# Optimization experiments

Measured on AMD Instinct MI355X. Metric: run time of the kernel, lower is better.

Reference implementation:

```python
import jax, jax.numpy as jnp
import numpy as np
import math

D_MODEL = 1024
NUM_HEADS = 16
SEQ = 2048
BATCH = 4


def setup_inputs() -> dict:
    key = jax.random.key(0)
    ks = jax.random.split(key, 7)
    s = 0.02
    return {
        "x": jax.random.normal(ks[0], (BATCH, SEQ, D_MODEL), jnp.float32),
        "Wq": jax.random.normal(ks[1], (D_MODEL, D_MODEL), jnp.float32) * s,
        "bq": jax.random.normal(ks[2], (D_MODEL,), jnp.float32) * s,
        "Wkv": jax.random.normal(ks[3], (D_MODEL, 2 * D_MODEL), jnp.float32) * s,
        "bkv": jax.random.normal(ks[4], (2 * D_MODEL,), jnp.float32) * s,
        "Wo": jax.random.normal(ks[5], (D_MODEL, D_MODEL), jnp.float32) * s,
        "bo": jax.random.normal(ks[6], (D_MODEL,), jnp.float32) * s,
        "decoderMask": 1,
    }


def reference(x, Wq, bq, Wkv, bkv, Wo, bo, decoderMask):
    B, S, D = x.shape
    H = NUM_HEADS
    dh = D // H
    q_ = x @ Wq + bq              # [B,S,D]
    kv_ = x @ Wkv + bkv           # [B,S,2D] (self-attention: m is None)
    # Faithful to source: concat [q_, kv_] then reshape into heads of 3*dh,
    # which interleaves Q/KV projection columns across heads.
    qkv = jnp.concatenate([q_, kv_], axis=-1)          # [B,S,3D]
    qkv = qkv.reshape(B, S, H, 3 * dh).transpose(0, 2, 1, 3)  # [B,H,S,3dh]
    q, k, v = jnp.split(qkv, 3, axis=-1)               # each [B,H,S,dh]
    scaled = jnp.einsum("bhqd,bhkd->bhqk", q, k) / math.sqrt(dh)
    if decoderMask:
        mask = jnp.triu(jnp.full((S, S), -jnp.inf, dtype=scaled.dtype), k=1)
        scaled = scaled + mask
    attn = jax.nn.softmax(scaled, axis=-1)
    vals = jnp.einsum("bhqk,bhkd->bhqd", attn, v)      # [B,H,S,dh]
    vals = vals.transpose(0, 2, 1, 3).reshape(B, S, D)
    return vals @ Wo + bo
```

## Files before the change

### kernel.cpp

```cpp
#include <hip/hip_runtime.h>
#include <cstddef>
#include <cstdint>

#define SEQ   2048
#define BATCH 4
#define DM    1024
#define NH    16
#define DH    64
#define ROWS  (BATCH*SEQ)
#define NC3   3072
#define SM_SCALE 0.18033688f

typedef unsigned short u16;
typedef __attribute__((ext_vector_type(8))) short bf16x8;
typedef __attribute__((ext_vector_type(2))) float f32x2;
typedef __attribute__((ext_vector_type(4))) float f32x4;
typedef __attribute__((ext_vector_type(16))) float f32x16;
typedef __attribute__((ext_vector_type(4))) unsigned u32x4;
typedef __attribute__((ext_vector_type(2))) unsigned u32x2;

union V16 { f32x16 v; f32x2 p[8]; };

__device__ __forceinline__ u16 f2b(float f) {
  union { float f; unsigned u; } v; v.f = f;
  unsigned r = v.u + 0x7fffu + ((v.u >> 16) & 1u);
  return (u16)(r >> 16);
}

__device__ __forceinline__ unsigned cvt_pk_bf16(float lo, float hi) {
  unsigned r;
  asm("v_cvt_pk_bf16_f32 %0, %1, %2" : "=v"(r) : "v"(lo), "v"(hi));
  return r;
}

__device__ __forceinline__ void plswap(unsigned& a, unsigned& b) {
  auto rr = __builtin_amdgcn_permlane32_swap((int)a, (int)b, false, false);
  a = (unsigned)rr[0];
  b = (unsigned)rr[1];
}

__device__ __forceinline__ float ex2(float x) { return __builtin_amdgcn_exp2f(x); }

__device__ __forceinline__ void gld16(const void* g, void* l) {
  __builtin_amdgcn_global_load_lds((const __attribute__((address_space(1))) void*)g,
                                   (__attribute__((address_space(3))) void*)l,
                                   16, 0, 0);
}

__global__ __launch_bounds__(256) void prep_tw_kernel(
    const float* __restrict__ x, const float* __restrict__ bq,
    const float* __restrict__ bkv, u16* __restrict__ xb, float* __restrict__ bc,
    const float* __restrict__ Wq, const float* __restrict__ Wkv,
    const float* __restrict__ Wo, u16* __restrict__ Wt)
{
  __shared__ float t_[32][33];
  const int tid = threadIdx.x;
  if (blockIdx.x < 8192) {
    int i = blockIdx.x * 256 + tid;
    int idx = i * 4;
    float4 v = *(const float4*)(x + idx);
    xb[idx + 0] = f2b(v.x);
    xb[idx + 1] = f2b(v.y);
    xb[idx + 2] = f2b(v.z);
    xb[idx + 3] = f2b(v.w);
    if (i < NC3) bc[i] = (i < DM) ? bq[i] : bkv[i - DM];
  } else {
    const int bid = blockIdx.x - 8192;
    const int n0 = (bid & 127) * 32, k0 = (bid >> 7) * 32;
    const int xcol = tid & 31, yrow = tid >> 5;
    #pragma unroll
    for (int it = 0; it < 4; ++it) {
      int k = k0 + yrow + it * 8;
      int n = n0 + xcol;
      float v;
      if (n < DM)           v = Wq[k * DM + n];
      else if (n < NC3)     v = Wkv[k * (2 * DM) + (n - DM)];
      else                  v = Wo[k * DM + (n - NC3)];
      t_[yrow + it * 8][xcol] = v;
    }
    __syncthreads();
    #pragma unroll
    for (int it = 0; it < 4; ++it) {
      int n = n0 + yrow + it * 8;
      int k = k0 + xcol;
      Wt[(size_t)n * DM + k] = f2b(t_[xcol][yrow + it * 8]);
    }
  }
}

template <int MODE>
__global__ __launch_bounds__(256) void gemm_bt(
    const u16* __restrict__ A, const u16* __restrict__ Bt,
    const float* __restrict__ bias, void* __restrict__ C,
    u16* __restrict__ Vt, int M, int N, int K)
{
  __shared__ alignas(16) u16 lds_[3 * 8192];
  const int tid = threadIdx.x;
  const int lane = tid & 63, wid = tid >> 6;
  const int wr = (wid >> 1) * 64, wc = (wid & 1) * 64;
  const int l15 = lane & 15, lhi = lane >> 4;

  const int bid = blockIdx.x;
  const int xcd = bid & 7, t = bid >> 3;
  const int rsub = t & 7, colb = t >> 3;
  const int row0 = (xcd * 8 + rsub) * 128, col0 = colb * 128;
  const int sr = tid >> 2, scol = (tid & 3) * 8;

  const u16* aS0 = A  + (size_t)(row0 + sr) * K + scol;
  const u16* aS1 = A  + (size_t)(row0 + 64 + sr) * K + scol;
  const u16* bS0 = Bt + (size_t)(col0 + sr) * K + scol;
  const u16* bS1 = Bt + (size_t)(col0 + 64 + sr) * K + scol;
  const int dA = tid * 8;

  int aoff[4], boff[4];
  #pragma unroll
  for (int m = 0; m < 4; ++m) aoff[m] = (wr + m * 16 + l15) * 32 + lhi * 8;
  #pragma unroll
  for (int n = 0; n < 4; ++n) boff[n] = 4096 + (wc + n * 16 + l15) * 32 + lhi * 8;

  f32x4 acc[4][4];
  #pragma unroll
  for (int m = 0; m < 4; ++m)
    #pragma unroll
    for (int n = 0; n < 4; ++n) { f32x4 z = {0.f, 0.f, 0.f, 0.f}; acc[m][n] = z; }

  const int KT = K >> 5;

  auto stage = [&](int kt, u16* base) {
    const int ka = kt * 32;
    gld16(aS0 + ka, base + dA);
    gld16(aS1 + ka, base + 2048 + dA);
    gld16(bS0 + ka, base + 4096 + dA);
    gld16(bS1 + ka, base + 6144 + dA);
  };

  u16* const bufA = lds_;
  u16* const bufB = lds_ + 8192;
  u16* const bufC = lds_ + 16384;

  stage(0, bufA); stage(1, bufB);
  asm volatile("s_waitcnt vmcnt(4)" ::: "memory");
  __builtin_amdgcn_s_barrier();

  u16* rb = bufA;
  u16* sb = bufC;
  for (int kt = 0; kt < KT; ++kt) {
    bf16x8 a[4], b[4];
    #pragma unroll
    for (int m = 0; m < 4; ++m) a[m] = *(const bf16x8*)&rb[aoff[m]];
    #pragma unroll
    for (int n = 0; n < 4; ++n) b[n] = *(const bf16x8*)&rb[boff[n]];
    if (kt + 2 < KT) stage(kt + 2, sb);
    __builtin_amdgcn_s_setprio(1);
    #pragma unroll
    for (int m = 0; m < 4; ++m)
      #pragma unroll
      for (int n = 0; n < 4; ++n)
        acc[m][n] = __builtin_amdgcn_mfma_f32_16x16x32_bf16(a[m], b[n], acc[m][n], 0, 0, 0);
    __builtin_amdgcn_s_setprio(0);
    if (kt + 1 < KT) {
      if (kt + 2 < KT) { asm volatile("s_waitcnt vmcnt(4)" ::: "memory"); }
      else             { asm volatile("s_waitcnt vmcnt(0)" ::: "memory"); }
      __builtin_amdgcn_s_barrier();
    }
    rb = (rb == bufC) ? bufA : rb + 8192;
    sb = (sb == bufC) ? bufA : sb + 8192;
  }

  #pragma unroll
  for (int m = 0; m < 4; ++m)
    #pragma unroll
    for (int n = 0; n < 4; ++n) {
      const int col = col0 + wc + n * 16 + l15;
      const float bv = bias[col];
      if (MODE == 0) {
        #pragma unroll
        for (int r = 0; r < 4; ++r) {
          const int row = row0 + wr + m * 16 + lhi * 4 + r;
          ((float*)C)[(size_t)row * N + col] = acc[m][n][r] + bv;
        }
      } else {
        const int hh = col / 192;
        const int cc = col - hh * 192;
        if (cc < 128) {
          const float qs = (cc < 64) ? SM_SCALE : 1.f;
          #pragma unroll
          for (int r = 0; r < 4; ++r) {
            const int row = row0 + wr + m * 16 + lhi * 4 + r;
            ((u16*)C)[(size_t)row * N + col] = f2b((acc[m][n][r] + bv) * qs);
          }
        } else {
          u16 wv[4];
          #pragma unroll
          for (int r = 0; r < 4; ++r) wv[r] = f2b(acc[m][n][r] + bv);
          const int row = row0 + wr + m * 16 + lhi * 4;
          const int bb = row >> 11, j = row & (SEQ - 1);
          u16* vt = Vt + ((size_t)(bb * NH + hh) * 64 + (cc - 128)) * SEQ + j;
          u32x2 pv = { (unsigned)wv[0] | ((unsigned)wv[1] << 16),
                       (unsigned)wv[2] | ((unsigned)wv[3] << 16) };
          *(u32x2*)vt = pv;
        }
      }
    }
}

__global__ __launch_bounds__(256) void attn_kernel(
    const u16* __restrict__ qkv, const u16* __restrict__ Vt, u16* __restrict__ ctx)
{
  const int bid = blockIdx.x;
  const int p   = (bid >> 3) & 7;
  const int g   = (bid & 7) + ((bid >> 6) << 3);
  const int h   = g & 15, b = g >> 4;
  const int tid = threadIdx.x;
  const int lane = tid & 63, wid = tid >> 6;
  const int l31 = lane & 31, lhi5 = lane >> 5;

  __shared__ alignas(16) u16 smem[8192 + 3 * 8192];
  u16* const Qs = smem;
  u16* const R0 = smem + 8192;
  u16* const R1 = R0 + 8192;
  u16* const R2 = R1 + 8192;

  const size_t kv_row = (size_t)(b * NH + h) * 64;
  const int sr = tid >> 3, sck = tid & 7;
  const int scks = sck ^ (sr & 7);

  const u16* kBase = qkv + (size_t)(b * SEQ + sr) * NC3 + h * 192 + 64 + scks * 8;
  const u16* vBase = Vt + (kv_row + sr) * SEQ + scks * 8;
  const size_t kRow32 = (size_t)32 * NC3;
  const size_t vRow32 = (size_t)32 * SEQ;
  const int dOff0 = sr * 64 + sck * 8;
  const int dOff1 = (32 + sr) * 64 + sck * 8;

  int koff[4], koff2[4];
  #pragma unroll
  for (int c = 0; c < 4; ++c) {
    koff[c]  = l31 * 64        + (((2 * c + lhi5) ^ (l31 & 7)) * 8);
    koff2[c] = (32 + l31) * 64 + (((2 * c + lhi5) ^ (l31 & 7)) * 8);
  }

  #pragma unroll 1
  for (int half = 0; half < 2; ++half) {
    const int qt = half ? (7 - p) : (8 + p);
    const int q0 = qt * 128;
    const int nt = qt * 2 + 2;

    #pragma unroll
    for (int it = 0; it < 4; ++it) {
      int row = it * 32 + sr;
      gld16(qkv + (size_t)(b * SEQ + q0 + row) * NC3 + h * 192 + scks * 8,
            Qs + row * 64 + sck * 8);
    }
    {
      const u16* ks = kBase;          const u16* vs = vBase;
      gld16(ks,          R0 + dOff0); gld16(ks + kRow32, R0 + dOff1);
      gld16(vs,          R0 + 4096 + dOff0); gld16(vs + vRow32, R0 + 4096 + dOff1);
      ks = kBase + (size_t)64 * NC3;  vs = vBase + 64;
      gld16(ks,          R1 + dOff0); gld16(ks + kRow32, R1 + dOff1);
      gld16(vs,          R1 + 4096 + dOff0); gld16(vs + vRow32, R1 + 4096 + dOff1);
    }
    asm volatile("s_waitcnt vmcnt(4)" ::: "memory");
    __builtin_amdgcn_s_barrier();

    bf16x8 qf[4];
    {
      const int qrow = wid * 32 + l31;
      #pragma unroll
      for (int c = 0; c < 4; ++c)
        qf[c] = *(const bf16x8*)&Qs[qrow * 64 + (((2 * c + lhi5) ^ (qrow & 7)) * 8)];
    }

    V16 o0, o1;
    #pragma unroll
    for (int r = 0; r < 16; ++r) { o0.v[r] = 0.f; o1.v[r] = 0.f; }
    float lrow = 0.f;

    const int qw0 = q0 + wid * 32;
    const int qa  = qw0 + l31;
    const int dqb = qa - 4 * lhi5;

    u16* rb = R0;
    u16* sb = R2;
    for (int jt = 0; jt < nt; ++jt) {
      const int j0 = jt * 64;

      if (jt + 2 < nt) {
        const u16* ks = kBase + (size_t)(j0 + 128) * NC3;
        const u16* vs = vBase + (j0 + 128);
        gld16(ks,          sb + dOff0); gld16(ks + kRow32, sb + dOff1);
        gld16(vs,          sb + 4096 + dOff0); gld16(vs + vRow32, sb + 4096 + dOff1);
      }

      if (j0 <= qw0 + 31) {
        const u16* Kb = rb;
        const u16* Vb = rb + 4096;
        V16 s0, s1;
        #pragma unroll
        for (int r = 0; r < 16; ++r) { s0.v[r] = 0.f; s1.v[r] = 0.f; }
        __builtin_amdgcn_s_setprio(1);
        #pragma unroll
        for (int c = 0; c < 4; ++c) {
          bf16x8 kf = *(const bf16x8*)&Kb[koff[c]];
          s0.v = __builtin_amdgcn_mfma_f32_32x32x16_bf16(kf, qf[c], s0.v, 0, 0, 0);
        }
        #pragma unroll
        for (int c = 0; c < 4; ++c) {
          bf16x8 kf = *(const bf16x8*)&Kb[koff2[c]];
          s1.v = __builtin_amdgcn_mfma_f32_32x32x16_bf16(kf, qf[c], s1.v, 0, 0, 0);
        }
        __builtin_amdgcn_s_setprio(0);

        if (j0 + 63 > qw0) {
          const int dq = dqb - j0;
          #pragma unroll
          for (int r = 0; r < 16; ++r) {
            const int kvc = (r & 3) + 8 * (r >> 2);
            s0.v[r] = (kvc > dq)      ? -1e30f : s0.v[r];
            s1.v[r] = (kvc + 32 > dq) ? -1e30f : s1.v[r];
          }
        }

        f32x2 sum2 = {0.f, 0.f};
        #pragma unroll
        for (int i = 0; i < 8; ++i) {
          f32x2 e0, e1;
          e0[0] = ex2(s0.p[i][0]); e0[1] = ex2(s0.p[i][1]);
          e1[0] = ex2(s1.p[i][0]); e1[1] = ex2(s1.p[i][1]);
          s0.p[i] = e0; s1.p[i] = e1;
          sum2 += e0 + e1;
        }
        float ps = sum2[0] + sum2[1];
        {
          unsigned a = __builtin_bit_cast(unsigned, ps), bb = a;
          plswap(a, bb);
          ps = __builtin_bit_cast(float, a) + __builtin_bit_cast(float, bb);
        }
        lrow += ps;

        unsigned pk0[8], pk1[8];
        #pragma unroll
        for (int i = 0; i < 4; ++i) {
          pk0[2 * i]     = cvt_pk_bf16(s0.v[4 * i + 0], s0.v[4 * i + 1]);
          pk0[2 * i + 1] = cvt_pk_bf16(s0.v[4 * i + 2], s0.v[4 * i + 3]);
          pk1[2 * i]     = cvt_pk_bf16(s1.v[4 * i + 0], s1.v[4 * i + 1]);
          pk1[2 * i + 1] = cvt_pk_bf16(s1.v[4 * i + 2], s1.v[4 * i + 3]);
        }
        bf16x8 pf[4];
        {
          unsigned a0 = pk0[0], b0 = pk0[2]; plswap(a0, b0);
          unsigned a1 = pk0[1], b1 = pk0[3]; plswap(a1, b1);
          u32x4 w0v = {a0, a1, b0, b1}; pf[0] = __builtin_bit_cast(bf16x8, w0v);
          unsigned a2 = pk0[4], b2 = pk0[6]; plswap(a2, b2);
          unsigned a3 = pk0[5], b3 = pk0[7]; plswap(a3, b3);
          u32x4 w1v = {a2, a3, b2, b3}; pf[1] = __builtin_bit_cast(bf16x8, w1v);
          unsigned a4 = pk1[0], b4 = pk1[2]; plswap(a4, b4);
          unsigned a5 = pk1[1], b5 = pk1[3]; plswap(a5, b5);
          u32x4 w2v = {a4, a5, b4, b5}; pf[2] = __builtin_bit_cast(bf16x8, w2v);
          unsigned a6 = pk1[4], b6 = pk1[6]; plswap(a6, b6);
          unsigned a7 = pk1[5], b7 = pk1[7]; plswap(a7, b7);
          u32x4 w3v = {a6, a7, b6, b7}; pf[3] = __builtin_bit_cast(bf16x8, w3v);
        }

        __builtin_amdgcn_s_setprio(1);
        #pragma unroll
        for (int c = 0; c < 4; ++c) {
          bf16x8 vf = *(const bf16x8*)&Vb[koff[c]];
          o0.v = __builtin_amdgcn_mfma_f32_32x32x16_bf16(vf, pf[c], o0.v, 0, 0, 0);
        }
        #pragma unroll
        for (int c = 0; c < 4; ++c) {
          bf16x8 vf = *(const bf16x8*)&Vb[koff2[c]];
          o1.v = __builtin_amdgcn_mfma_f32_32x32x16_bf16(vf, pf[c], o1.v, 0, 0, 0);
        }
        __builtin_amdgcn_s_setprio(0);
      }

      if (jt + 2 < nt)      { asm volatile("s_waitcnt vmcnt(4)" ::: "memory"); }
      else if (jt + 1 < nt) { asm volatile("s_waitcnt vmcnt(0)" ::: "memory"); }
      __builtin_amdgcn_s_barrier();
      rb = (rb == R2) ? R0 : rb + 8192;
      sb = (sb == R2) ? R0 : sb + 8192;
    }

    const float inv = 1.f / lrow;
    u16* crow = ctx + (size_t)(b * SEQ + qa) * DM + h * DH;
    #pragma unroll
    for (int i = 0; i < 4; ++i) {
      u32x2 v0, v1;
      v0[0] = cvt_pk_bf16(o0.v[4 * i + 0] * inv, o0.v[4 * i + 1] * inv);
      v0[1] = cvt_pk_bf16(o0.v[4 * i + 2] * inv, o0.v[4 * i + 3] * inv);
      v1[0] = cvt_pk_bf16(o1.v[4 * i + 0] * inv, o1.v[4 * i + 1] * inv);
      v1[1] = cvt_pk_bf16(o1.v[4 * i + 2] * inv, o1.v[4 * i + 3] * inv);
      *(u32x2*)&crow[8 * i + 4 * lhi5]      = v0;
      *(u32x2*)&crow[32 + 8 * i + 4 * lhi5] = v1;
    }
  }
}

extern "C" void kernel_launch(void* const* d_in, const int* in_sizes, int n_in,
                              void* d_out, int out_size, void* d_ws, size_t ws_size,
                              hipStream_t stream) {
  (void)in_sizes; (void)n_in; (void)out_size; (void)ws_size;
  const float* x   = (const float*)d_in[0];
  const float* Wq  = (const float*)d_in[1];
  const float* bq  = (const float*)d_in[2];
  const float* Wkv = (const float*)d_in[3];
  const float* bkv = (const float*)d_in[4];
  const float* Wo  = (const float*)d_in[5];
  const float* bo  = (const float*)d_in[6];
  float* out = (float*)d_out;

  char* w = (char*)d_ws;
  size_t off = 0;
  auto alloc = [&](size_t bytes) { void* p = w + off; off += (bytes + 255) & ~(size_t)255; return p; };
  u16*   xb   = (u16*)alloc((size_t)ROWS * DM * 2);
  u16*   qkvb = (u16*)alloc((size_t)ROWS * NC3 * 2);
  u16*   Vt   = (u16*)alloc((size_t)BATCH * NH * DH * SEQ * 2);
  u16*   Wt   = (u16*)alloc((size_t)4096 * DM * 2);
  float* bc   = (float*)alloc((size_t)NC3 * 4);
  u16*   ctx  = xb;

  prep_tw_kernel<<<dim3(8192 + 4096), 256, 0, stream>>>(x, bq, bkv, xb, bc, Wq, Wkv, Wo, Wt);
  gemm_bt<1><<<dim3((ROWS / 128) * (NC3 / 128)), 256, 0, stream>>>(xb, Wt, bc, qkvb, Vt, ROWS, NC3, DM);
  attn_kernel<<<dim3(512), 256, 0, stream>>>(qkvb, Vt, ctx);
  gemm_bt<0><<<dim3((ROWS / 128) * (DM / 128)), 256, 0, stream>>>(ctx, Wt + (size_t)NC3 * DM, bo, out, nullptr, ROWS, DM, DM);
}
```

Before: 162.3 us.

## Software-pipeline QK^T one tile ahead with a four-deep K/V ring

Grows the LDS K/V ring from three to four stages and prefetches three tiles ahead. It also computes the next tile's QK^T scores before the current tile's softmax and PV MFMAs, so matrix work can overlap the exp and pack instructions. The goal is to hide global-load latency and the dependency stall between score MFMAs and softmax. In exchange it uses more LDS, which may cut occupancy, and holds extra score registers, which may raise VGPR pressure.

```diff
diff --git a/kernel.cpp b/kernel.cpp
--- a/kernel.cpp
+++ b/kernel.cpp
@@ -215,11 +215,9 @@
   const int lane = tid & 63, wid = tid >> 6;
   const int l31 = lane & 31, lhi5 = lane >> 5;
 
-  __shared__ alignas(16) u16 smem[8192 + 3 * 8192];
-  u16* const Qs = smem;
-  u16* const R0 = smem + 8192;
-  u16* const R1 = R0 + 8192;
-  u16* const R2 = R1 + 8192;
+  __shared__ alignas(16) u16 smem[8192 + 4 * 8192];
+  u16* const Qs   = smem;
+  u16* const Ring = smem + 8192;
 
   const size_t kv_row = (size_t)(b * NH + h) * 64;
   const int sr = tid >> 3, sck = tid & 7;
@@ -239,6 +237,16 @@
     koff2[c] = (32 + l31) * 64 + (((2 * c + lhi5) ^ (l31 & 7)) * 8);
   }
 
+  auto stageKV = [&](int jt) {
+    u16* base = Ring + (jt & 3) * 8192;
+    const u16* ks = kBase + (size_t)(jt * 64) * NC3;
+    const u16* vs = vBase + jt * 64;
+    gld16(ks,          base + dOff0);
+    gld16(ks + kRow32, base + dOff1);
+    gld16(vs,          base + 4096 + dOff0);
+    gld16(vs + vRow32, base + 4096 + dOff1);
+  };
+
   #pragma unroll 1
   for (int half = 0; half < 2; ++half) {
     const int qt = half ? (7 - p) : (8 + p);
@@ -251,15 +259,9 @@
       gld16(qkv + (size_t)(b * SEQ + q0 + row) * NC3 + h * 192 + scks * 8,
             Qs + row * 64 + sck * 8);
     }
-    {
-      const u16* ks = kBase;          const u16* vs = vBase;
-      gld16(ks,          R0 + dOff0); gld16(ks + kRow32, R0 + dOff1);
-      gld16(vs,          R0 + 4096 + dOff0); gld16(vs + vRow32, R0 + 4096 + dOff1);
-      ks = kBase + (size_t)64 * NC3;  vs = vBase + 64;
-      gld16(ks,          R1 + dOff0); gld16(ks + kRow32, R1 + dOff1);
-      gld16(vs,          R1 + 4096 + dOff0); gld16(vs + vRow32, R1 + 4096 + dOff1);
-    }
-    asm volatile("s_waitcnt vmcnt(4)" ::: "memory");
+    stageKV(0); stageKV(1);
+    if (nt > 2) { stageKV(2); asm volatile("s_waitcnt vmcnt(4)" ::: "memory"); }
+    else        {             asm volatile("s_waitcnt vmcnt(0)" ::: "memory"); }
     __builtin_amdgcn_s_barrier();
 
     bf16x8 qf[4];
@@ -270,6 +272,25 @@
         qf[c] = *(const bf16x8*)&Qs[qrow * 64 + (((2 * c + lhi5) ^ (qrow & 7)) * 8)];
     }
 
+    auto qkt = [&](const u16* Kb, V16& s0o, V16& s1o) {
+      V16 s0, s1;
+      #pragma unroll
+      for (int r = 0; r < 16; ++r) { s0.v[r] = 0.f; s1.v[r] = 0.f; }
+      __builtin_amdgcn_s_setprio(1);
+      #pragma unroll
+      for (int c = 0; c < 4; ++c) {
+        bf16x8 kf = *(const bf16x8*)&Kb[koff[c]];
+        s0.v = __builtin_amdgcn_mfma_f32_32x32x16_bf16(kf, qf[c], s0.v, 0, 0, 0);
+      }
+      #pragma unroll
+      for (int c = 0; c < 4; ++c) {
+        bf16x8 kf = *(const bf16x8*)&Kb[koff2[c]];
+        s1.v = __builtin_amdgcn_mfma_f32_32x32x16_bf16(kf, qf[c], s1.v, 0, 0, 0);
+      }
+      __builtin_amdgcn_s_setprio(0);
+      s0o = s0; s1o = s1;
+    };
+
     V16 o0, o1;
     #pragma unroll
     for (int r = 0; r < 16; ++r) { o0.v[r] = 0.f; o1.v[r] = 0.f; }
@@ -279,44 +300,27 @@
     const int qa  = qw0 + l31;
     const int dqb = qa - 4 * lhi5;
 
-    u16* rb = R0;
-    u16* sb = R2;
+    V16 sc0, sc1;
+    qkt(Ring, sc0, sc1);
+
+    #pragma unroll 1
     for (int jt = 0; jt < nt; ++jt) {
       const int j0 = jt * 64;
 
-      if (jt + 2 < nt) {
-        const u16* ks = kBase + (size_t)(j0 + 128) * NC3;
-        const u16* vs = vBase + (j0 + 128);
-        gld16(ks,          sb + dOff0); gld16(ks + kRow32, sb + dOff1);
-        gld16(vs,          sb + 4096 + dOff0); gld16(vs + vRow32, sb + 4096 + dOff1);
-      }
+      if (jt + 3 < nt) stageKV(jt + 3);
+
+      V16 sn0, sn1;
+      const bool haveNext = (jt + 1 < nt) && (j0 + 64 <= qw0 + 31);
+      if (haveNext) qkt(Ring + ((jt + 1) & 3) * 8192, sn0, sn1);
 
       if (j0 <= qw0 + 31) {
-        const u16* Kb = rb;
-        const u16* Vb = rb + 4096;
-        V16 s0, s1;
-        #pragma unroll
-        for (int r = 0; r < 16; ++r) { s0.v[r] = 0.f; s1.v[r] = 0.f; }
-        __builtin_amdgcn_s_setprio(1);
-        #pragma unroll
-        for (int c = 0; c < 4; ++c) {
-          bf16x8 kf = *(const bf16x8*)&Kb[koff[c]];
-          s0.v = __builtin_amdgcn_mfma_f32_32x32x16_bf16(kf, qf[c], s0.v, 0, 0, 0);
-        }
-        #pragma unroll
-        for (int c = 0; c < 4; ++c) {
-          bf16x8 kf = *(const bf16x8*)&Kb[koff2[c]];
-          s1.v = __builtin_amdgcn_mfma_f32_32x32x16_bf16(kf, qf[c], s1.v, 0, 0, 0);
-        }
-        __builtin_amdgcn_s_setprio(0);
-
         if (j0 + 63 > qw0) {
           const int dq = dqb - j0;
           #pragma unroll
           for (int r = 0; r < 16; ++r) {
             const int kvc = (r & 3) + 8 * (r >> 2);
-            s0.v[r] = (kvc > dq)      ? -1e30f : s0.v[r];
-            s1.v[r] = (kvc + 32 > dq) ? -1e30f : s1.v[r];
+            sc0.v[r] = (kvc > dq)      ? -1e30f : sc0.v[r];
+            sc1.v[r] = (kvc + 32 > dq) ? -1e30f : sc1.v[r];
           }
         }
 
@@ -324,9 +328,9 @@
         #pragma unroll
         for (int i = 0; i < 8; ++i) {
           f32x2 e0, e1;
-          e0[0] = ex2(s0.p[i][0]); e0[1] = ex2(s0.p[i][1]);
-          e1[0] = ex2(s1.p[i][0]); e1[1] = ex2(s1.p[i][1]);
-          s0.p[i] = e0; s1.p[i] = e1;
+          e0[0] = ex2(sc0.p[i][0]); e0[1] = ex2(sc0.p[i][1]);
+          e1[0] = ex2(sc1.p[i][0]); e1[1] = ex2(sc1.p[i][1]);
+          sc0.p[i] = e0; sc1.p[i] = e1;
           sum2 += e0 + e1;
         }
         float ps = sum2[0] + sum2[1];
@@ -340,10 +344,10 @@
         unsigned pk0[8], pk1[8];
         #pragma unroll
         for (int i = 0; i < 4; ++i) {
-          pk0[2 * i]     = cvt_pk_bf16(s0.v[4 * i + 0], s0.v[4 * i + 1]);
-          pk0[2 * i + 1] = cvt_pk_bf16(s0.v[4 * i + 2], s0.v[4 * i + 3]);
-          pk1[2 * i]     = cvt_pk_bf16(s1.v[4 * i + 0], s1.v[4 * i + 1]);
-          pk1[2 * i + 1] = cvt_pk_bf16(s1.v[4 * i + 2], s1.v[4 * i + 3]);
+          pk0[2 * i]     = cvt_pk_bf16(sc0.v[4 * i + 0], sc0.v[4 * i + 1]);
+          pk0[2 * i + 1] = cvt_pk_bf16(sc0.v[4 * i + 2], sc0.v[4 * i + 3]);
+          pk1[2 * i]     = cvt_pk_bf16(sc1.v[4 * i + 0], sc1.v[4 * i + 1]);
+          pk1[2 * i + 1] = cvt_pk_bf16(sc1.v[4 * i + 2], sc1.v[4 * i + 3]);
         }
         bf16x8 pf[4];
         {
@@ -361,6 +365,7 @@
           u32x4 w3v = {a6, a7, b6, b7}; pf[3] = __builtin_bit_cast(bf16x8, w3v);
         }
 
+        const u16* Vb = Ring + (jt & 3) * 8192 + 4096;
         __builtin_amdgcn_s_setprio(1);
         #pragma unroll
         for (int c = 0; c < 4; ++c) {
@@ -375,11 +380,11 @@
         __builtin_amdgcn_s_setprio(0);
       }
 
-      if (jt + 2 < nt)      { asm volatile("s_waitcnt vmcnt(4)" ::: "memory"); }
-      else if (jt + 1 < nt) { asm volatile("s_waitcnt vmcnt(0)" ::: "memory"); }
+      if (jt + 3 < nt)      { asm volatile("s_waitcnt vmcnt(4)" ::: "memory"); }
+      else if (jt + 2 < nt) { asm volatile("s_waitcnt vmcnt(0)" ::: "memory"); }
       __builtin_amdgcn_s_barrier();
-      rb = (rb == R2) ? R0 : rb + 8192;
-      sb = (sb == R2) ? R0 : sb + 8192;
+
+      if (haveNext) { sc0 = sn0; sc1 = sn1; }
     }
 
     const float inv = 1.f / lrow;
```

After: 215.2 us. 1.33x slower.
